# Performance work log

Hardware: AMD Instinct MI355X
Metric: run time of the kernel (lower is better)

The kernel has to match this reference:

```python
import jax, jax.numpy as jnp
import numpy as np

B, S, D = 2, 2048, 2048
N_HEADS, N_KV_HEADS, HEAD_DIM = 16, 8, 128
N_REP = N_HEADS // N_KV_HEADS
EPS = 1e-6
SCALE = HEAD_DIM ** -0.5


def setup_inputs() -> dict:
    key = jax.random.key(0)
    ks = jax.random.split(key, 6)
    x = jax.random.normal(ks[0], (B, S, D), dtype=jnp.float32)
    # RoPE frequencies (Llama-style cis stored as interleaved [cos, sin])
    inv_freq = 1.0 / (1e6 ** (jnp.arange(0, HEAD_DIM, 2, dtype=jnp.float32) / HEAD_DIM))
    angles = jnp.arange(S, dtype=jnp.float32)[:, None] * inv_freq[None, :]  # [S, HEAD_DIM//2]
    freqs_cis = jnp.stack([jnp.cos(angles), jnp.sin(angles)], axis=-1)  # [S, HEAD_DIM//2, 2]
    wq = jax.random.normal(ks[1], (N_HEADS * HEAD_DIM, D), dtype=jnp.float32) * 0.02
    wk = jax.random.normal(ks[2], (N_KV_HEADS * HEAD_DIM, D), dtype=jnp.float32) * 0.02
    wv = jax.random.normal(ks[3], (N_KV_HEADS * HEAD_DIM, D), dtype=jnp.float32) * 0.02
    wo = jax.random.normal(ks[4], (D, N_HEADS * HEAD_DIM), dtype=jnp.float32) * 0.02
    q_norm_w = jnp.ones((HEAD_DIM,), dtype=jnp.float32)
    k_norm_w = jnp.ones((HEAD_DIM,), dtype=jnp.float32)
    return {"x": x, "freqs_cis": freqs_cis, "wq": wq, "wk": wk, "wv": wv,
            "wo": wo, "q_norm_w": q_norm_w, "k_norm_w": k_norm_w}


def _rmsnorm(t, w):
    var = jnp.mean(jnp.square(t), axis=-1, keepdims=True)
    return t * jax.lax.rsqrt(var + EPS) * w


def _apply_rope(t, cos, sin):
    # t: [B, S, H, HEAD_DIM]; cos/sin: [1, S, 1, HEAD_DIM//2]
    tp = t.reshape(*t.shape[:-1], HEAD_DIM // 2, 2)
    tr, ti = tp[..., 0], tp[..., 1]
    out = jnp.stack([tr * cos - ti * sin, tr * sin + ti * cos], axis=-1)
    return out.reshape(t.shape)


def reference(x, freqs_cis, wq, wk, wv, wo, q_norm_w, k_norm_w):
    bs, seqlen, _ = x.shape
    xq = (x @ wq.T).reshape(bs, seqlen, N_HEADS, HEAD_DIM)
    xk = (x @ wk.T).reshape(bs, seqlen, N_KV_HEADS, HEAD_DIM)
    xv = (x @ wv.T).reshape(bs, seqlen, N_KV_HEADS, HEAD_DIM)
    # per-head RMSNorm (Qwen3)
    xq = _rmsnorm(xq, q_norm_w)
    xk = _rmsnorm(xk, k_norm_w)
    # rotary embedding
    cos = freqs_cis[:seqlen, :, 0][None, :, None, :]
    sin = freqs_cis[:seqlen, :, 1][None, :, None, :]
    xq = _apply_rope(xq, cos, sin)
    xk = _apply_rope(xk, cos, sin)
    # GQA: repeat kv heads
    keys = jnp.repeat(xk, N_REP, axis=2)    # [B, S, N_HEADS, HEAD_DIM]
    values = jnp.repeat(xv, N_REP, axis=2)
    q = xq.transpose(0, 2, 1, 3)   # [B, H, S, D]
    k = keys.transpose(0, 2, 1, 3)
    v = values.transpose(0, 2, 1, 3)
    scores = jnp.einsum("bhqd,bhkd->bhqk", q, k) * SCALE
    causal = jnp.tril(jnp.ones((seqlen, seqlen), dtype=bool))
    scores = jnp.where(causal[None, None], scores, jnp.finfo(scores.dtype).min)
    attn = jax.nn.softmax(scores, axis=-1)
    out = jnp.einsum("bhqk,bhkd->bhqd", attn, v)
    out = out.transpose(0, 2, 1, 3).reshape(bs, seqlen, N_HEADS * HEAD_DIM)
    return out @ wo.T
```

## Files before the change

### kernel.cpp

```cpp
#include <hip/hip_runtime.h>

#define B_ 2
#define S_ 2048
#define D_ 2048
#define NH 16
#define NKV 8
#define HD 128
#define SCALE 0.08838834764831845f
#define CEXP 0.1275255f
#define RTHR 62.733f

typedef unsigned short u16;
typedef __attribute__((ext_vector_type(8))) short short8;
typedef __attribute__((ext_vector_type(4))) float f32x4;
typedef __attribute__((ext_vector_type(16))) float f32x16;
typedef __attribute__((ext_vector_type(4))) int i32x4;
typedef __attribute__((ext_vector_type(2))) int i32x2;

#define ASM_VMCNT(N) asm volatile("s_waitcnt vmcnt(" #N ")" ::: "memory")
#define MEMFENCE asm volatile("" ::: "memory")

__device__ __forceinline__ u16 f2b(float f) {
  union { float f; unsigned u; } c; c.f = f;
  unsigned u = c.u;
  return (u16)((u + 0x7fffu + ((u >> 16) & 1u)) >> 16);
}
__device__ __forceinline__ float b2f(u16 h) {
  union { unsigned u; float f; } c; c.u = ((unsigned)h) << 16;
  return c.f;
}
__device__ __forceinline__ float exp2f_fast(float x) {
  float r; asm("v_exp_f32 %0, %1" : "=v"(r) : "v"(x)); return r;
}
__device__ __forceinline__ int cvtpk(float a, float b) {
  int r; asm("v_cvt_pk_bf16_f32 %0, %1, %2" : "=v"(r) : "v"(a), "v"(b)); return r;
}
__device__ __forceinline__ void pl32swap(int& a, int& b) {
  asm volatile("v_permlane32_swap_b32 %0, %1" : "+v"(a), "+v"(b));
}

__device__ __forceinline__ void load_lds16(const u16* g, u16* l) {
  __builtin_amdgcn_global_load_lds(
      (const __attribute__((address_space(1))) unsigned int*)g,
      (__attribute__((address_space(3))) unsigned int*)l, 16, 0, 0);
}

__global__ __launch_bounds__(256) void cvt_all(const float* __restrict__ x,
                                               const float* __restrict__ wq,
                                               const float* __restrict__ wk,
                                               const float* __restrict__ wv,
                                               const float* __restrict__ wo,
                                               u16* __restrict__ xb,
                                               u16* __restrict__ wqkvb,
                                               u16* __restrict__ wob) {
  const int blk = blockIdx.x;
  const float* src; u16* dst; int base;
  if (blk < 8192)       { src = x;  dst = xb;                  base = blk; }
  else if (blk < 12288) { src = wq; dst = wqkvb;               base = blk - 8192; }
  else if (blk < 14336) { src = wk; dst = wqkvb + 2048 * 2048; base = blk - 12288; }
  else if (blk < 16384) { src = wv; dst = wqkvb + 3072 * 2048; base = blk - 14336; }
  else                  { src = wo; dst = wob;                 base = blk - 16384; }
  int i = base * 256 + threadIdx.x;
  float4 v = ((const float4*)src)[i];
  u16 o0 = f2b(v.x), o1 = f2b(v.y), o2 = f2b(v.z), o3 = f2b(v.w);
  unsigned long long packed = (unsigned long long)o0 | ((unsigned long long)o1 << 16) |
                              ((unsigned long long)o2 << 32) | ((unsigned long long)o3 << 48);
  ((unsigned long long*)dst)[i] = packed;
}

#define LDA4Q(dst, SRC) \
  { _Pragma("unroll") for (int i2 = 0; i2 < 4; ++i2) { \
      const int arow = wr * 64 + i2 * 16 + r; \
      dst[i2] = *(const short8*)&(SRC)[arow * 32 + ((hi ^ ((arow >> 1) & 3)) << 3)]; } }
#define LDB4Q(dst, SRC) \
  { _Pragma("unroll") for (int n2 = 0; n2 < 4; ++n2) { \
      const int brow = wc * 64 + n2 * 16 + r; \
      dst[n2] = *(const short8*)&(SRC)[brow * 32 + ((hi ^ ((brow >> 1) & 3)) << 3)]; } }
#define MFMA16Q(AF, BF) \
  { __builtin_amdgcn_s_setprio(1); \
    _Pragma("unroll") for (int i2 = 0; i2 < 4; ++i2) \
    _Pragma("unroll") for (int n2 = 0; n2 < 4; ++n2) \
      acc[i2][n2] = __builtin_amdgcn_mfma_f32_16x16x32_bf16(AF[i2], BF[n2], acc[i2][n2], 0, 0, 0); \
    __builtin_amdgcn_s_setprio(0); }

__global__ __launch_bounds__(512, 4) void gemm256x128(const u16* __restrict__ A,
                                                      const u16* __restrict__ Bm,
                                                      u16* __restrict__ C) {
  __shared__ __align__(16) u16 As2[2][8192];
  __shared__ __align__(16) u16 Bs2[2][4096];
  const int tid = threadIdx.x;
  const int wave = tid >> 6, lane = tid & 63;
  const int L = (blockIdx.x & 7) * 64 + (blockIdx.x >> 3);
  const int bm = L >> 5, bn = L & 31;
  const int wr = wave >> 1, wc = wave & 1;
  const int r = lane & 15, hi = lane >> 4;
  const int rowA0 = bm * 256, rowB0 = bn * 128;

  f32x4 acc[4][4];
#pragma unroll
  for (int mi = 0; mi < 4; ++mi)
#pragma unroll
    for (int ni = 0; ni < 4; ++ni) acc[mi][ni] = (f32x4){0.f, 0.f, 0.f, 0.f};

  auto stage_ha = [&](u16* lds, int kcol) {
#pragma unroll
    for (int l = 0; l < 2; ++l) {
      const int p = wave * 2048 + l * 1024 + lane * 16;
      const int row = p >> 6, slot = (p >> 4) & 3;
      const int kg = slot ^ ((row >> 1) & 3);
      load_lds16(A + (size_t)(rowA0 + row) * 2048 + kcol + kg * 8,
                 lds + ((wave * 2048 + l * 1024) >> 1));
    }
  };
  auto stage_hb = [&](u16* lds, int kcol) {
    const int p = wave * 1024 + lane * 16;
    const int row = p >> 6, slot = (p >> 4) & 3;
    const int kg = slot ^ ((row >> 1) & 3);
    load_lds16(Bm + (size_t)(rowB0 + row) * 2048 + kcol + kg * 8,
               lds + ((wave * 1024) >> 1));
  };

  for (int kt = 0; kt < 32; ++kt) {
    const int k0 = kt << 6;
    stage_ha(As2[0], k0);
    stage_hb(Bs2[0], k0);
    stage_ha(As2[1], k0 + 32);
    stage_hb(Bs2[1], k0 + 32);
    ASM_VMCNT(0);
    __builtin_amdgcn_s_barrier();
    MEMFENCE;
    short8 af[4], bf[4];
    LDB4Q(bf, Bs2[0]); LDA4Q(af, As2[0]);
    MFMA16Q(af, bf);
    LDB4Q(bf, Bs2[1]); LDA4Q(af, As2[1]);
    MFMA16Q(af, bf);
    MEMFENCE;
    __builtin_amdgcn_s_barrier();
  }

#pragma unroll
  for (int mi = 0; mi < 4; ++mi)
#pragma unroll
    for (int ni = 0; ni < 4; ++ni)
#pragma unroll
      for (int r2 = 0; r2 < 4; ++r2) {
        int grow = bm * 256 + wr * 64 + mi * 16 + hi * 4 + r2;
        int gcol = bn * 128 + wc * 64 + ni * 16 + r;
        C[(size_t)grow * 4096 + gcol] = f2b(acc[mi][ni][r2]);
      }
}

template<int OUTF32>
__global__ __launch_bounds__(256, 2) void gemm_bt2(const u16* __restrict__ A, const u16* __restrict__ Bm,
                                                   void* __restrict__ Cv, int M, int N, int K, int nbn) {
  __shared__ __align__(16) u16 As[2][128 * 64];
  __shared__ __align__(16) u16 Bs[2][128 * 64];
  const int tid = threadIdx.x;
  const int wave = tid >> 6, lane = tid & 63;
  const int nwg = gridDim.x, cpx = nwg >> 3;
  const int L = (blockIdx.x & 7) * cpx + (blockIdx.x >> 3);
  const int bm = L / nbn, bn = L % nbn;
  const int wr = wave >> 1, wc = wave & 1;
  const int r = lane & 15, hi = lane >> 4;

  f32x4 acc[4][4];
#pragma unroll
  for (int m = 0; m < 4; ++m)
#pragma unroll
    for (int n = 0; n < 4; ++n) acc[m][n] = (f32x4){0.f, 0.f, 0.f, 0.f};

  const int gslot = (lane & 7) ^ (lane >> 3);
  const int srow = lane >> 3;

  auto stage = [&](int buf, int k0) {
#pragma unroll
    for (int jj = 0; jj < 4; ++jj) {
      int j = wave * 4 + jj;
      int row = j * 8 + srow;
      load_lds16(A + (size_t)(bm * 128 + row) * K + k0 + gslot * 8, &As[buf][j * 512]);
      load_lds16(Bm + (size_t)(bn * 128 + row) * K + k0 + gslot * 8, &Bs[buf][j * 512]);
    }
  };

  const int nk = K >> 6;
  stage(0, 0);
  for (int kt = 0; kt < nk; ++kt) {
    if (kt + 1 < nk) {
      stage((kt + 1) & 1, (kt + 1) << 6);
      ASM_VMCNT(8);
    } else {
      ASM_VMCNT(0);
    }
    __builtin_amdgcn_s_barrier();
    MEMFENCE;
    const u16* as = As[kt & 1];
    const u16* bs = Bs[kt & 1];
#pragma unroll
    for (int kc = 0; kc < 2; ++kc) {
      short8 af[4], bfr[4];
#pragma unroll
      for (int m = 0; m < 4; ++m) {
        int row = wr * 64 + m * 16 + r;
        int slot = (hi + kc * 4) ^ (row & 7);
        af[m] = *(const short8*)&as[row * 64 + slot * 8];
      }
#pragma unroll
      for (int n = 0; n < 4; ++n) {
        int row = wc * 64 + n * 16 + r;
        int slot = (hi + kc * 4) ^ (row & 7);
        bfr[n] = *(const short8*)&bs[row * 64 + slot * 8];
      }
#pragma unroll
      for (int m = 0; m < 4; ++m)
#pragma unroll
        for (int n = 0; n < 4; ++n)
          acc[m][n] = __builtin_amdgcn_mfma_f32_16x16x32_bf16(af[m], bfr[n], acc[m][n], 0, 0, 0);
    }
    MEMFENCE;
    __builtin_amdgcn_s_barrier();
  }

#pragma unroll
  for (int m = 0; m < 4; ++m)
#pragma unroll
    for (int n = 0; n < 4; ++n)
#pragma unroll
      for (int r2 = 0; r2 < 4; ++r2) {
        int grow = bm * 128 + wr * 64 + m * 16 + hi * 4 + r2;
        int gcol = bn * 128 + wc * 64 + n * 16 + r;
        if (OUTF32)
          ((float*)Cv)[(size_t)grow * N + gcol] = acc[m][n][r2];
        else
          ((u16*)Cv)[(size_t)grow * N + gcol] = f2b(acc[m][n][r2]);
      }
}

__global__ __launch_bounds__(256) void rmsnorm_rope(const u16* __restrict__ qkv, const float* __restrict__ fc,
                                                    const float* __restrict__ qw, const float* __restrict__ kw,
                                                    u16* __restrict__ qr, u16* __restrict__ kr) {
  const int tid = threadIdx.x, wave = tid >> 6, lane = tid & 63;
  const int rowid = blockIdx.x * 4 + wave;
  const int token = rowid / 24;
  const int hh = rowid % 24;
  const int b = token >> 11, s = token & 2047;
  const bool isq = hh < 16;
  const int off = isq ? hh * 128 : 2048 + (hh - 16) * 128;
  const u16* src = qkv + (size_t)token * 4096 + off + lane * 2;
  unsigned pv = *(const unsigned*)src;
  float t0 = b2f((u16)(pv & 0xffffu));
  float t1 = b2f((u16)(pv >> 16));
  float ss = t0 * t0 + t1 * t1;
#pragma unroll
  for (int mm = 1; mm < 64; mm <<= 1) ss += __shfl_xor(ss, mm, 64);
  float rms = rsqrtf(ss * (1.0f / 128.0f) + 1e-6f);
  const float* nw = isq ? qw : kw;
  t0 *= rms * nw[lane * 2];
  t1 *= rms * nw[lane * 2 + 1];
  float c = fc[(s * 64 + lane) * 2], sn = fc[(s * 64 + lane) * 2 + 1];
  float o0 = t0 * c - t1 * sn;
  float o1 = t0 * sn + t1 * c;
  unsigned ov = (unsigned)f2b(o0) | ((unsigned)f2b(o1) << 16);
  if (isq)
    *(unsigned*)(qr + ((size_t)(b * 16 + hh) * 2048 + s) * 128 + lane * 2) = ov;
  else
    *(unsigned*)(kr + ((size_t)(b * 8 + hh - 16) * 2048 + s) * 128 + lane * 2) = ov;
}

__global__ __launch_bounds__(256) void v_transpose(const u16* __restrict__ qkv, u16* __restrict__ vt) {
  __shared__ __align__(16) u16 tile[64][136];
  const int blk = blockIdx.x;
  const int st = blk & 31, h = (blk >> 5) & 7, b = blk >> 8;
  const int s0 = st * 64, t = threadIdx.x;
#pragma unroll
  for (int p = 0; p < 4; ++p) {
    int row = p * 16 + (t >> 4), c8 = (t & 15) * 8;
    const u16* src = qkv + (size_t)(b * 2048 + s0 + row) * 4096 + 3072 + h * 128 + c8;
    *(short8*)&tile[row][c8] = *(const short8*)src;
  }
  __syncthreads();
  const int d = t >> 1, j0 = (t & 1) * 32;
  u16* dst = vt + ((size_t)(b * 8 + h) * 128 + d) * 2048 + s0 + j0;
#pragma unroll
  for (int j = 0; j < 32; j += 8) {
    short8 v;
#pragma unroll
    for (int u = 0; u < 8; ++u) v[u] = (short)tile[j0 + j + u][d];
    *(short8*)(dst + j) = v;
  }
}

__global__ __launch_bounds__(256, 2) void attn7(const u16* __restrict__ qr, const u16* __restrict__ kr,
                                                const u16* __restrict__ vt, u16* __restrict__ ao) {
  __shared__ __align__(16) u16 Ks[2][64 * 128];
  __shared__ __align__(16) u16 Vs[2][128 * 64];
  const int tid = threadIdx.x, wave = tid >> 6, lane = tid & 63;
  const int ql = lane & 31, lh = lane >> 5;

  const int blk = blockIdx.x;
  const int half = blk >> 8;
  const int xcd = blk & 7;
  const int idx = (blk >> 3) & 31;
  const int bh = xcd * 4 + (idx & 3);
  const int pp = idx >> 2;
  const int t = half ? pp : 15 - pp;
  const int b = bh >> 4, h = bh & 15, hkv = h >> 1;

  const u16* Q  = qr + (size_t)(b * 16 + h) * S_ * HD;
  const u16* Kg = kr + (size_t)(b * 8 + hkv) * S_ * HD;
  const u16* Vg = vt + (size_t)(b * 8 + hkv) * HD * S_;

  const int q0w = t * 128 + wave * 32;
  const int nsteps = 2 * (t + 1);

  short8 qf[8];
#pragma unroll
  for (int ki = 0; ki < 8; ++ki)
    qf[ki] = *(const short8*)(Q + (size_t)(q0w + ql) * HD + ki * 16 + lh * 8);

  f32x16 o[4];
#pragma unroll
  for (int dt = 0; dt < 4; ++dt) o[dt] = 0.f;
  float m = -1e30f, l = 0.f;

  auto stage = [&](int buf, int kv0) {
#pragma unroll
    for (int inst = 0; inst < 4; ++inst) {
      int pp2 = wave * 4096 + inst * 1024 + lane * 16;
      int row = pp2 >> 8;
      int colb = (pp2 & 255) ^ ((row & 7) << 4);
      load_lds16(Kg + (((size_t)(kv0 + row)) << 7) + (colb >> 1),
                 &Ks[buf][(wave * 4096 + inst * 1024) >> 1]);
    }
#pragma unroll
    for (int inst = 0; inst < 4; ++inst) {
      int pp2 = wave * 4096 + inst * 1024 + lane * 16;
      int d = pp2 >> 7;
      int colb = (pp2 & 127) ^ ((d & 7) << 4);
      load_lds16(Vg + (size_t)d * S_ + kv0 + (colb >> 1),
                 &Vs[buf][(wave * 4096 + inst * 1024) >> 1]);
    }
  };

  stage(0, 0);
  for (int i = 0; i < nsteps; ++i) {
    const int kv0 = i * 64;
    const u16* kb = Ks[i & 1];
    const u16* vb = Vs[i & 1];
    if (i + 1 < nsteps) {
      stage((i + 1) & 1, kv0 + 64);
      ASM_VMCNT(8);
    } else {
      ASM_VMCNT(0);
    }
    __builtin_amdgcn_s_barrier();
    MEMFENCE;

    if (kv0 < q0w + 32) {
      f32x16 sacc[2];
      sacc[0] = 0.f; sacc[1] = 0.f;
      __builtin_amdgcn_s_setprio(1);
#pragma unroll
      for (int ki = 0; ki < 8; ++ki) {
        const int off = ki * 32 + lh * 16;
#pragma unroll
        for (int kvt = 0; kvt < 2; ++kvt) {
          const int row = kvt * 32 + ql;
          short8 kf = *(const short8*)&kb[(row << 7) + ((off ^ ((row & 7) << 4)) >> 1)];
          sacc[kvt] = __builtin_amdgcn_mfma_f32_32x32x16_bf16(kf, qf[ki], sacc[kvt], 0, 0, 0);
        }
      }
      __builtin_amdgcn_s_setprio(0);
      const int q = q0w + ql;
      if (kv0 + 64 > q0w) {
#pragma unroll
        for (int kvt = 0; kvt < 2; ++kvt) {
          const int kvb = kv0 + kvt * 32 + 4 * lh;
#pragma unroll
          for (int reg = 0; reg < 16; ++reg) {
            const int kvr = kvb + (reg & 3) + 8 * (reg >> 2);
            sacc[kvt][reg] = (kvr > q) ? -1e30f : sacc[kvt][reg];
          }
        }
      }
      float mx = sacc[0][0];
#pragma unroll
      for (int kvt = 0; kvt < 2; ++kvt)
#pragma unroll
        for (int reg = 0; reg < 16; ++reg) mx = fmaxf(mx, sacc[kvt][reg]);
      mx = fmaxf(mx, __shfl_xor(mx, 32, 64));
      if (__any(mx > m + RTHR)) {
        float mn = fmaxf(m, mx);
        float sc = exp2f_fast((m - mn) * CEXP);
        l *= sc;
        m = mn;
#pragma unroll
        for (int dt = 0; dt < 4; ++dt)
#pragma unroll
          for (int reg = 0; reg < 16; ++reg) o[dt][reg] *= sc;
      }
      short8 pf[4];
      const float mc = m * CEXP;
      float ps = 0.f;
#pragma unroll
      for (int kvt = 0; kvt < 2; ++kvt) {
        float pv[16];
#pragma unroll
        for (int reg = 0; reg < 16; ++reg) {
          pv[reg] = exp2f_fast(__builtin_fmaf(sacc[kvt][reg], CEXP, -mc));
          ps += pv[reg];
        }
        int A0 = cvtpk(pv[0], pv[1]),  B0 = cvtpk(pv[2], pv[3]);
        int C0 = cvtpk(pv[4], pv[5]),  D0 = cvtpk(pv[6], pv[7]);
        int A1 = cvtpk(pv[8], pv[9]),  B1 = cvtpk(pv[10], pv[11]);
        int C1 = cvtpk(pv[12], pv[13]), D1 = cvtpk(pv[14], pv[15]);
        pl32swap(A0, C0);
        pl32swap(B0, D0);
        pl32swap(A1, C1);
        pl32swap(B1, D1);
        i32x4 w0 = (i32x4){A0, B0, C0, D0};
        i32x4 w1 = (i32x4){A1, B1, C1, D1};
        pf[kvt * 2]     = *(short8*)&w0;
        pf[kvt * 2 + 1] = *(short8*)&w1;
      }
      l += ps;
      __builtin_amdgcn_s_setprio(1);
#pragma unroll
      for (int kc = 0; kc < 4; ++kc) {
        const int off = kc * 32 + lh * 16;
#pragma unroll
        for (int dt = 0; dt < 4; ++dt) {
          const int d = dt * 32 + ql;
          short8 vf = *(const short8*)&vb[(d << 6) + ((off ^ ((d & 7) << 4)) >> 1)];
          o[dt] = __builtin_amdgcn_mfma_f32_32x32x16_bf16(vf, pf[kc], o[dt], 0, 0, 0);
        }
      }
      __builtin_amdgcn_s_setprio(0);
    }
    MEMFENCE;
    __builtin_amdgcn_s_barrier();
  }

  l += __shfl_xor(l, 32, 64);
  const float inv = 1.0f / l;
  const size_t rowoff = ((size_t)(b * 2048 + q0w + ql)) * 2048 + h * 128;
#pragma unroll
  for (int dt = 0; dt < 4; ++dt)
#pragma unroll
    for (int g = 0; g < 4; ++g) {
      const int d0 = dt * 32 + 8 * g + 4 * lh;
      int w0 = cvtpk(o[dt][4 * g] * inv, o[dt][4 * g + 1] * inv);
      int w1 = cvtpk(o[dt][4 * g + 2] * inv, o[dt][4 * g + 3] * inv);
      i32x2 pk = (i32x2){w0, w1};
      *(i32x2*)((u16*)ao + rowoff + d0) = pk;
    }
}

extern "C" void kernel_launch(void* const* d_in, const int* in_sizes, int n_in,
                              void* d_out, int out_size, void* d_ws, size_t ws_size,
                              hipStream_t stream) {
  const float* x = (const float*)d_in[0];
  const float* fc = (const float*)d_in[1];
  const float* wq = (const float*)d_in[2];
  const float* wk = (const float*)d_in[3];
  const float* wv = (const float*)d_in[4];
  const float* wo = (const float*)d_in[5];
  const float* qw = (const float*)d_in[6];
  const float* kw = (const float*)d_in[7];
  float* out = (float*)d_out;
  char* ws = (char*)d_ws;

  u16* xb    = (u16*)(ws);
  u16* wqkvb = (u16*)(ws + 16777216);
  u16* wob   = (u16*)(ws + 33554432);
  u16* qkv   = (u16*)(ws + 41943040);
  u16* qrope = (u16*)(ws + 75497472);
  u16* krope = (u16*)(ws + 92274688);
  u16* vtb   = (u16*)(ws + 100663296);
  u16* ao    = (u16*)(ws + 109051904);

  cvt_all<<<20480, 256, 0, stream>>>(x, wq, wk, wv, wo, xb, wqkvb, wob);

  gemm256x128<<<512, 512, 0, stream>>>(xb, wqkvb, qkv);

  rmsnorm_rope<<<24576, 256, 0, stream>>>(qkv, fc, qw, kw, qrope, krope);
  v_transpose<<<512, 256, 0, stream>>>(qkv, vtb);

  attn7<<<512, 256, 0, stream>>>(qrope, krope, vtb, ao);

  gemm_bt2<1><<<512, 256, 0, stream>>>(ao, wob, (void*)out, 4096, 2048, 2048, 16);
}
```

Measured before the change: 209.5 us.

## Process two 32-row query groups per wave in attention, halving waves per block

The attention kernel now runs 2 waves per block instead of 4. Each wave handles 64 query rows as two 32-row groups, so every K and V fragment read from LDS feeds two MFMAs and LDS read traffic per unit of work drops. Staging loads are redistributed over fewer waves, and the vmcnt wait is raised to match. The costs are roughly double the accumulator and Q registers per wave, less latency hiding with fewer waves per CU, and coarser causal skipping, since a wave only skips a KV tile when all 64 of its rows are past it.

```diff
diff --git a/kernel.cpp b/kernel.cpp
--- a/kernel.cpp
+++ b/kernel.cpp
@@ -289,7 +289,7 @@
   }
 }
 
-__global__ __launch_bounds__(256, 2) void attn7(const u16* __restrict__ qr, const u16* __restrict__ kr,
+__global__ __launch_bounds__(128, 1) void attn8(const u16* __restrict__ qr, const u16* __restrict__ kr,
                                                 const u16* __restrict__ vt, u16* __restrict__ ao) {
   __shared__ __align__(16) u16 Ks[2][64 * 128];
   __shared__ __align__(16) u16 Vs[2][128 * 64];
@@ -309,35 +309,37 @@
   const u16* Kg = kr + (size_t)(b * 8 + hkv) * S_ * HD;
   const u16* Vg = vt + (size_t)(b * 8 + hkv) * HD * S_;
 
-  const int q0w = t * 128 + wave * 32;
+  const int q0w = t * 128 + wave * 64;
   const int nsteps = 2 * (t + 1);
 
-  short8 qf[8];
+  short8 qf[8][2];
 #pragma unroll
   for (int ki = 0; ki < 8; ++ki)
-    qf[ki] = *(const short8*)(Q + (size_t)(q0w + ql) * HD + ki * 16 + lh * 8);
-
-  f32x16 o[4];
-#pragma unroll
-  for (int dt = 0; dt < 4; ++dt) o[dt] = 0.f;
-  float m = -1e30f, l = 0.f;
+#pragma unroll
+    for (int qg = 0; qg < 2; ++qg)
+      qf[ki][qg] = *(const short8*)(Q + (size_t)(q0w + qg * 32 + ql) * HD + ki * 16 + lh * 8);
+
+  f32x16 o[4][2];
+#pragma unroll
+  for (int dt = 0; dt < 4; ++dt) { o[dt][0] = 0.f; o[dt][1] = 0.f; }
+  float m[2] = {-1e30f, -1e30f}, l[2] = {0.f, 0.f};
 
   auto stage = [&](int buf, int kv0) {
 #pragma unroll
-    for (int inst = 0; inst < 4; ++inst) {
-      int pp2 = wave * 4096 + inst * 1024 + lane * 16;
-      int row = pp2 >> 8;
-      int colb = (pp2 & 255) ^ ((row & 7) << 4);
+    for (int inst = 0; inst < 8; ++inst) {
+      int p = inst * 2048 + wave * 1024 + lane * 16;
+      int row = p >> 8;
+      int colb = (p & 255) ^ ((row & 7) << 4);
       load_lds16(Kg + (((size_t)(kv0 + row)) << 7) + (colb >> 1),
-                 &Ks[buf][(wave * 4096 + inst * 1024) >> 1]);
-    }
-#pragma unroll
-    for (int inst = 0; inst < 4; ++inst) {
-      int pp2 = wave * 4096 + inst * 1024 + lane * 16;
-      int d = pp2 >> 7;
-      int colb = (pp2 & 127) ^ ((d & 7) << 4);
+                 &Ks[buf][(inst * 2048 + wave * 1024) >> 1]);
+    }
+#pragma unroll
+    for (int inst = 0; inst < 8; ++inst) {
+      int p = inst * 2048 + wave * 1024 + lane * 16;
+      int d = p >> 7;
+      int colb = (p & 127) ^ ((d & 7) << 4);
       load_lds16(Vg + (size_t)d * S_ + kv0 + (colb >> 1),
-                 &Vs[buf][(wave * 4096 + inst * 1024) >> 1]);
+                 &Vs[buf][(inst * 2048 + wave * 1024) >> 1]);
     }
   };
 
@@ -348,16 +350,16 @@
     const u16* vb = Vs[i & 1];
     if (i + 1 < nsteps) {
       stage((i + 1) & 1, kv0 + 64);
-      ASM_VMCNT(8);
+      ASM_VMCNT(16);
     } else {
       ASM_VMCNT(0);
     }
     __builtin_amdgcn_s_barrier();
     MEMFENCE;
 
-    if (kv0 < q0w + 32) {
-      f32x16 sacc[2];
-      sacc[0] = 0.f; sacc[1] = 0.f;
+    if (kv0 < q0w + 64) {
+      f32x16 sacc[2][2];
+      sacc[0][0] = 0.f; sacc[0][1] = 0.f; sacc[1][0] = 0.f; sacc[1][1] = 0.f;
       __builtin_amdgcn_s_setprio(1);
 #pragma unroll
       for (int ki = 0; ki < 8; ++ki) {
@@ -366,63 +368,79 @@
         for (int kvt = 0; kvt < 2; ++kvt) {
           const int row = kvt * 32 + ql;
           short8 kf = *(const short8*)&kb[(row << 7) + ((off ^ ((row & 7) << 4)) >> 1)];
-          sacc[kvt] = __builtin_amdgcn_mfma_f32_32x32x16_bf16(kf, qf[ki], sacc[kvt], 0, 0, 0);
+          sacc[kvt][0] = __builtin_amdgcn_mfma_f32_32x32x16_bf16(kf, qf[ki][0], sacc[kvt][0], 0, 0, 0);
+          sacc[kvt][1] = __builtin_amdgcn_mfma_f32_32x32x16_bf16(kf, qf[ki][1], sacc[kvt][1], 0, 0, 0);
         }
       }
       __builtin_amdgcn_s_setprio(0);
-      const int q = q0w + ql;
       if (kv0 + 64 > q0w) {
 #pragma unroll
-        for (int kvt = 0; kvt < 2; ++kvt) {
-          const int kvb = kv0 + kvt * 32 + 4 * lh;
-#pragma unroll
-          for (int reg = 0; reg < 16; ++reg) {
-            const int kvr = kvb + (reg & 3) + 8 * (reg >> 2);
-            sacc[kvt][reg] = (kvr > q) ? -1e30f : sacc[kvt][reg];
+        for (int qg = 0; qg < 2; ++qg) {
+          const int q = q0w + qg * 32 + ql;
+#pragma unroll
+          for (int kvt = 0; kvt < 2; ++kvt) {
+            const int kvb = kv0 + kvt * 32 + 4 * lh;
+#pragma unroll
+            for (int reg = 0; reg < 16; ++reg) {
+              const int kvr = kvb + (reg & 3) + 8 * (reg >> 2);
+              sacc[kvt][qg][reg] = (kvr > q) ? -1e30f : sacc[kvt][qg][reg];
+            }
           }
         }
       }
-      float mx = sacc[0][0];
-#pragma unroll
-      for (int kvt = 0; kvt < 2; ++kvt)
-#pragma unroll
-        for (int reg = 0; reg < 16; ++reg) mx = fmaxf(mx, sacc[kvt][reg]);
-      mx = fmaxf(mx, __shfl_xor(mx, 32, 64));
-      if (__any(mx > m + RTHR)) {
-        float mn = fmaxf(m, mx);
-        float sc = exp2f_fast((m - mn) * CEXP);
-        l *= sc;
-        m = mn;
-#pragma unroll
-        for (int dt = 0; dt < 4; ++dt)
-#pragma unroll
-          for (int reg = 0; reg < 16; ++reg) o[dt][reg] *= sc;
-      }
-      short8 pf[4];
-      const float mc = m * CEXP;
-      float ps = 0.f;
-#pragma unroll
-      for (int kvt = 0; kvt < 2; ++kvt) {
-        float pv[16];
-#pragma unroll
-        for (int reg = 0; reg < 16; ++reg) {
-          pv[reg] = exp2f_fast(__builtin_fmaf(sacc[kvt][reg], CEXP, -mc));
-          ps += pv[reg];
+      float mx[2];
+#pragma unroll
+      for (int qg = 0; qg < 2; ++qg) {
+        float v = sacc[0][qg][0];
+#pragma unroll
+        for (int kvt = 0; kvt < 2; ++kvt)
+#pragma unroll
+          for (int reg = 0; reg < 16; ++reg) v = fmaxf(v, sacc[kvt][qg][reg]);
+        v = fmaxf(v, __shfl_xor(v, 32, 64));
+        mx[qg] = v;
+      }
+      bool need = (mx[0] > m[0] + RTHR) || (mx[1] > m[1] + RTHR);
+      if (__any(need)) {
+#pragma unroll
+        for (int qg = 0; qg < 2; ++qg) {
+          float mn = fmaxf(m[qg], mx[qg]);
+          float sc = exp2f_fast((m[qg] - mn) * CEXP);
+          l[qg] *= sc;
+          m[qg] = mn;
+#pragma unroll
+          for (int dt = 0; dt < 4; ++dt)
+#pragma unroll
+            for (int reg = 0; reg < 16; ++reg) o[dt][qg][reg] *= sc;
         }
-        int A0 = cvtpk(pv[0], pv[1]),  B0 = cvtpk(pv[2], pv[3]);
-        int C0 = cvtpk(pv[4], pv[5]),  D0 = cvtpk(pv[6], pv[7]);
-        int A1 = cvtpk(pv[8], pv[9]),  B1 = cvtpk(pv[10], pv[11]);
-        int C1 = cvtpk(pv[12], pv[13]), D1 = cvtpk(pv[14], pv[15]);
-        pl32swap(A0, C0);
-        pl32swap(B0, D0);
-        pl32swap(A1, C1);
-        pl32swap(B1, D1);
-        i32x4 w0 = (i32x4){A0, B0, C0, D0};
-        i32x4 w1 = (i32x4){A1, B1, C1, D1};
-        pf[kvt * 2]     = *(short8*)&w0;
-        pf[kvt * 2 + 1] = *(short8*)&w1;
-      }
-      l += ps;
+      }
+      short8 pf[4][2];
+#pragma unroll
+      for (int qg = 0; qg < 2; ++qg) {
+        const float mc = m[qg] * CEXP;
+        float ps = 0.f;
+#pragma unroll
+        for (int kvt = 0; kvt < 2; ++kvt) {
+          float pv[16];
+#pragma unroll
+          for (int reg = 0; reg < 16; ++reg) {
+            pv[reg] = exp2f_fast(__builtin_fmaf(sacc[kvt][qg][reg], CEXP, -mc));
+            ps += pv[reg];
+          }
+          int A0 = cvtpk(pv[0], pv[1]),  B0 = cvtpk(pv[2], pv[3]);
+          int C0 = cvtpk(pv[4], pv[5]),  D0 = cvtpk(pv[6], pv[7]);
+          int A1 = cvtpk(pv[8], pv[9]),  B1 = cvtpk(pv[10], pv[11]);
+          int C1 = cvtpk(pv[12], pv[13]), D1 = cvtpk(pv[14], pv[15]);
+          pl32swap(A0, C0);
+          pl32swap(B0, D0);
+          pl32swap(A1, C1);
+          pl32swap(B1, D1);
+          i32x4 w0 = (i32x4){A0, B0, C0, D0};
+          i32x4 w1 = (i32x4){A1, B1, C1, D1};
+          pf[kvt * 2][qg]     = *(short8*)&w0;
+          pf[kvt * 2 + 1][qg] = *(short8*)&w1;
+        }
+        l[qg] += ps;
+      }
       __builtin_amdgcn_s_setprio(1);
 #pragma unroll
       for (int kc = 0; kc < 4; ++kc) {
@@ -431,7 +449,8 @@
         for (int dt = 0; dt < 4; ++dt) {
           const int d = dt * 32 + ql;
           short8 vf = *(const short8*)&vb[(d << 6) + ((off ^ ((d & 7) << 4)) >> 1)];
-          o[dt] = __builtin_amdgcn_mfma_f32_32x32x16_bf16(vf, pf[kc], o[dt], 0, 0, 0);
+          o[dt][0] = __builtin_amdgcn_mfma_f32_32x32x16_bf16(vf, pf[kc][0], o[dt][0], 0, 0, 0);
+          o[dt][1] = __builtin_amdgcn_mfma_f32_32x32x16_bf16(vf, pf[kc][1], o[dt][1], 0, 0, 0);
         }
       }
       __builtin_amdgcn_s_setprio(0);
@@ -440,19 +459,23 @@
     __builtin_amdgcn_s_barrier();
   }
 
-  l += __shfl_xor(l, 32, 64);
-  const float inv = 1.0f / l;
-  const size_t rowoff = ((size_t)(b * 2048 + q0w + ql)) * 2048 + h * 128;
-#pragma unroll
-  for (int dt = 0; dt < 4; ++dt)
-#pragma unroll
-    for (int g = 0; g < 4; ++g) {
-      const int d0 = dt * 32 + 8 * g + 4 * lh;
-      int w0 = cvtpk(o[dt][4 * g] * inv, o[dt][4 * g + 1] * inv);
-      int w1 = cvtpk(o[dt][4 * g + 2] * inv, o[dt][4 * g + 3] * inv);
-      i32x2 pk = (i32x2){w0, w1};
-      *(i32x2*)((u16*)ao + rowoff + d0) = pk;
-    }
+#pragma unroll
+  for (int qg = 0; qg < 2; ++qg) {
+    float lt = l[qg];
+    lt += __shfl_xor(lt, 32, 64);
+    const float inv = 1.0f / lt;
+    const size_t rowoff = ((size_t)(b * 2048 + q0w + qg * 32 + ql)) * 2048 + h * 128;
+#pragma unroll
+    for (int dt = 0; dt < 4; ++dt)
+#pragma unroll
+      for (int g = 0; g < 4; ++g) {
+        const int d0 = dt * 32 + 8 * g + 4 * lh;
+        int w0 = cvtpk(o[dt][qg][4 * g] * inv, o[dt][qg][4 * g + 1] * inv);
+        int w1 = cvtpk(o[dt][qg][4 * g + 2] * inv, o[dt][qg][4 * g + 3] * inv);
+        i32x2 pk = (i32x2){w0, w1};
+        *(i32x2*)((u16*)ao + rowoff + d0) = pk;
+      }
+  }
 }
 
 extern "C" void kernel_launch(void* const* d_in, const int* in_sizes, int n_in,
@@ -485,7 +508,7 @@
   rmsnorm_rope<<<24576, 256, 0, stream>>>(qkv, fc, qw, kw, qrope, krope);
   v_transpose<<<512, 256, 0, stream>>>(qkv, vtb);
 
-  attn7<<<512, 256, 0, stream>>>(qrope, krope, vtb, ao);
+  attn8<<<512, 128, 0, stream>>>(qrope, krope, vtb, ao);
 
   gemm_bt2<1><<<512, 256, 0, stream>>>(ao, wob, (void*)out, 4096, 2048, 2048, 16);
 }
```

Result: slower. 248.3 us (+18.5%).
